# Performance work log

Hardware: AMD Instinct MI355X
Metric: run time of the kernel (lower is better)

The kernel has to match this reference:

```python
import jax, jax.numpy as jnp
import numpy as np

B, F, H, C, K = 4096, 1536, 256, 38, 7  # nodes, feat_dim(effnet_b3), hidden, classes, knn k
EPS = 1e-5  # BatchNorm eps


def setup_inputs() -> dict:
    key = jax.random.key(0)
    ks = jax.random.split(key, 20)
    r = lambda i, shape, s=1.0: jax.random.normal(ks[i], shape, jnp.float32) * s
    u = lambda i, shape: jax.random.uniform(ks[i], shape, jnp.float32, 0.5, 1.5)
    inp = {
        "features": r(0, (B, F)),          # CNN backbone output
        "noise": r(1, (B, B)),             # tie-break noise (scaled by 1e-6 inside)
        # BatchNorm1d on CNN features (eval mode: running stats)
        "bnf_g": jnp.ones((F,)), "bnf_b": jnp.zeros((F,)),
        "bnf_m": r(2, (F,), 0.1), "bnf_v": u(3, (F,)),
        # GCNConv weights
        "W1": r(4, (F, H), 0.02), "b1": jnp.zeros((H,)),
        "W2": r(5, (H, H), 0.05), "b2": jnp.zeros((H,)),
        "W3": r(6, (H, H), 0.05), "b3": jnp.zeros((H,)),
        # PyG BatchNorms (eval mode)
        "bn1_g": jnp.ones((H,)), "bn1_b": jnp.zeros((H,)), "bn1_m": r(7, (H,), 0.1), "bn1_v": u(8, (H,)),
        "bn2_g": jnp.ones((H,)), "bn2_b": jnp.zeros((H,)), "bn2_m": r(9, (H,), 0.1), "bn2_v": u(10, (H,)),
        "bn3_g": jnp.ones((H,)), "bn3_b": jnp.zeros((H,)), "bn3_m": r(11, (H,), 0.1), "bn3_v": u(12, (H,)),
        # classifier MLP
        "Wc1": r(13, (H + F, H // 2), 0.02), "bc1": jnp.zeros((H // 2,)),
        "Wc2": r(14, (H // 2, C), 0.05), "bc2": jnp.zeros((C,)),
    }
    return inp


def _bn(x, g, b, m, v):
    return (x - m) * jax.lax.rsqrt(v + EPS) * g + b


def _knn_edges(x, noise):
    # torch.cdist (p=2) + 1e-6 noise + topk smallest; drop self (col 0)
    sq = jnp.sum(x * x, axis=1)
    d2 = jnp.maximum(sq[:, None] + sq[None, :] - 2.0 * (x @ x.T), 0.0)
    d = jnp.sqrt(d2) + noise * 1e-6
    _, idx = jax.lax.top_k(-d, K + 1)          # smallest K+1 distances
    knn = idx[:, 1:]                           # [B, K] neighbors (col 0 = self)
    src = jnp.repeat(jnp.arange(B), K)         # edge i -> j as in edge_list [[i, j]]
    dst = knn.reshape(-1)
    return src, dst


def _gcn(x, src, dst, W, b):
    # GCNConv: add self-loops, symmetric normalization, aggregate at target (dst)
    h = x @ W
    loop = jnp.arange(B)
    s = jnp.concatenate([src, loop])
    t = jnp.concatenate([dst, loop])
    deg = jnp.zeros((B,), x.dtype).at[t].add(1.0)
    dinv = jax.lax.rsqrt(deg)                  # deg >= 1 due to self-loops
    norm = dinv[s] * dinv[t]
    out = jnp.zeros_like(h).at[t].add(norm[:, None] * h[s])
    return out + b


def reference(features, noise, bnf_g, bnf_b, bnf_m, bnf_v,
              W1, b1, W2, b2, W3, b3,
              bn1_g, bn1_b, bn1_m, bn1_v,
              bn2_g, bn2_b, bn2_m, bn2_v,
              bn3_g, bn3_b, bn3_m, bn3_v,
              Wc1, bc1, Wc2, bc2):
    # CNN head: BN (eval) + dropout(identity in eval)
    x = _bn(features, bnf_g, bnf_b, bnf_m, bnf_v)
    src, dst = _knn_edges(jax.lax.stop_gradient(x), noise)
    x_orig = x
    h = jax.nn.relu(_bn(_gcn(x, src, dst, W1, b1), bn1_g, bn1_b, bn1_m, bn1_v))
    h = jax.nn.relu(_bn(_gcn(h, src, dst, W2, b2), bn2_g, bn2_b, bn2_m, bn2_v))
    h = _bn(_gcn(h, src, dst, W3, b3), bn3_g, bn3_b, bn3_m, bn3_v)
    # batch = arange(B) => global_mean_pool is identity per node
    comb = jnp.concatenate([h, x_orig], axis=1)        # [B, H+F]
    hid = jax.nn.relu(comb @ Wc1 + bc1)
    return hid @ Wc2 + bc2                             # [B, num_classes]
```

## Files before the change

### kernel.cpp

```cpp
#include <hip/hip_runtime.h>
#include <hip/hip_bf16.h>
#include <math.h>

#define Bn 4096
#define Fn 1536
#define Hn 256
#define Cn 38
#define Kn 7
#define GBK 64

typedef __attribute__((ext_vector_type(8))) short short8;
typedef __attribute__((ext_vector_type(4))) float f32x4;
typedef unsigned long long u64;
typedef unsigned int u32;
typedef unsigned short u16;

__device__ __forceinline__ void gld16(const void* g, void* l) {
  __builtin_amdgcn_global_load_lds((const __attribute__((address_space(1))) unsigned int*)g,
                                   (__attribute__((address_space(3))) unsigned int*)l, 16, 0, 0);
}

__global__ void k_prep(const float* __restrict__ g, const float* __restrict__ b,
                       const float* __restrict__ m, const float* __restrict__ v,
                       double* __restrict__ A64, double* __restrict__ C64) {
  int f = blockIdx.x * 256 + threadIdx.x;
  if (f < Fn) {
    double rs = 1.0 / sqrt((double)v[f] + 1e-5);
    double a = (double)g[f] * rs;
    A64[f] = a;
    C64[f] = (double)b[f] - (double)m[f] * a;
  }
}

__global__ void k_bnsplit(const float* __restrict__ feat, const double* __restrict__ A64,
                          const double* __restrict__ C64,
                          u16* __restrict__ Ah, u16* __restrict__ Al) {
  int row = blockIdx.x;
  int f0 = threadIdx.x * 8;
  const float* fr = feat + (size_t)row * Fn + f0;
  float4 a = *reinterpret_cast<const float4*>(fr);
  float4 b = *reinterpret_cast<const float4*>(fr + 4);
  float xs[8] = {a.x, a.y, a.z, a.w, b.x, b.y, b.z, b.w};
  short8 hv, lv;
#pragma unroll
  for (int k = 0; k < 8; k++) {
    float x = (float)fma((double)xs[k], A64[f0 + k], C64[f0 + k]);
    __hip_bfloat16 h = __float2bfloat16(x);
    float hf = __bfloat162float(h);
    __hip_bfloat16 lo = __float2bfloat16(x - hf);
    hv[k] = (short)*reinterpret_cast<u16*>(&h);
    lv[k] = (short)*reinterpret_cast<u16*>(&lo);
  }
  *reinterpret_cast<short8*>(Ah + (size_t)row * Fn + f0) = hv;
  *reinterpret_cast<short8*>(Al + (size_t)row * Fn + f0) = lv;
}

__global__ void k_rowsq(const float* __restrict__ feat, const double* __restrict__ A64,
                        const double* __restrict__ C64, double* __restrict__ sq) {
  int row = blockIdx.x, tid = threadIdx.x;
  const float* fr = feat + (size_t)row * Fn;
  double s = 0.0;
  for (int f = tid; f < Fn; f += 256) {
    double x = fma((double)fr[f], A64[f], C64[f]);
    s += x * x;
  }
  for (int o = 32; o > 0; o >>= 1) s += __shfl_down(s, o);
  __shared__ double red[4];
  if ((tid & 63) == 0) red[tid >> 6] = s;
  __syncthreads();
  if (tid == 0) sq[row] = red[0] + red[1] + red[2] + red[3];
}

__global__ void k_wsplit(const float* __restrict__ W, int K, int N,
                         u16* __restrict__ Wth, u16* __restrict__ Wtl) {
  __shared__ float t[32][33];
  int k0 = blockIdx.y * 32, n0 = blockIdx.x * 32;
  int tx = threadIdx.x & 31, ty = threadIdx.x >> 5;
  for (int p = 0; p < 32; p += 8) {
    int k = k0 + ty + p, n = n0 + tx;
    t[ty + p][tx] = (k < K && n < N) ? W[(size_t)k * N + n] : 0.f;
  }
  __syncthreads();
  for (int p = 0; p < 32; p += 8) {
    int n = n0 + ty + p, k = k0 + tx;
    if (n < N && k < K) {
      float x = t[tx][ty + p];
      __hip_bfloat16 h = __float2bfloat16(x);
      float hf = __bfloat162float(h);
      __hip_bfloat16 lo = __float2bfloat16(x - hf);
      Wth[(size_t)n * K + k] = *reinterpret_cast<u16*>(&h);
      Wtl[(size_t)n * K + k] = *reinterpret_cast<u16*>(&lo);
    }
  }
}

__global__ __launch_bounds__(256) void k_gram(
    const u16* __restrict__ Ah, const double* __restrict__ sq, u64* __restrict__ part) {
  __shared__ union {
    u16 t[2][8192];
    float c2[128 * 65];
  } lds;
  const int tid = threadIdx.x;
  const int w = tid >> 6, l = tid & 63;
  int swz = (blockIdx.x & 7) * 66 + (blockIdx.x >> 3);
  int rem = swz, ti = 0;
#pragma unroll 1
  while (rem >= 32 - ti) { rem -= 32 - ti; ti++; }
  const int tj = ti + rem;
  const int rA0 = ti * 128, rB0 = tj * 128;
  const int isDiag = (ti == tj);

  f32x4 acc[4][4];
  const f32x4 fz = {0.f, 0.f, 0.f, 0.f};
#pragma unroll
  for (int i = 0; i < 4; i++)
#pragma unroll
    for (int j = 0; j < 4; j++) acc[i][j] = fz;

  const u16* mats[2] = { Ah + (size_t)rA0 * Fn, Ah + (size_t)rB0 * Fn };

  auto stage = [&](int k0) {
#pragma unroll
    for (int q = 0; q < 8; q++) {
      int idx = w * 8 + q;
      int mm = idx >> 4, kh = (idx >> 3) & 1, s = idx & 7;
      int row = s * 16 + (l >> 2);
      int colel = ((l & 3) * 8) ^ ((row & 8) ? 16 : 0);
      gld16(mats[mm] + (size_t)row * Fn + k0 + kh * 32 + colel,
            (char*)&lds.t[mm][0] + kh * 8192 + s * 1024);
    }
  };

  const int swzr = (l & 8) ? 32 : 0;
  const int cB = ((l >> 4) * 16) ^ swzr;

  stage(0);
  const int NT = Fn / GBK;
  for (int kt = 0; kt < NT; kt++) {
    __syncthreads();
#pragma unroll
    for (int kh = 0; kh < 2; kh++) {
      short8 fa[4], fb[4];
#pragma unroll
      for (int i = 0; i < 4; i++) {
        int ar = (w >> 1) * 64 + i * 16 + (l & 15);
        fa[i] = *reinterpret_cast<const short8*>((const char*)&lds.t[0][0] + kh * 8192 + ar * 64 + cB);
        int br = (w & 1) * 64 + i * 16 + (l & 15);
        fb[i] = *reinterpret_cast<const short8*>((const char*)&lds.t[1][0] + kh * 8192 + br * 64 + cB);
      }
#pragma unroll
      for (int i = 0; i < 4; i++)
#pragma unroll
        for (int j = 0; j < 4; j++)
          acc[i][j] = __builtin_amdgcn_mfma_f32_16x16x32_bf16(fa[i], fb[j], acc[i][j], 0, 0, 0);
    }
    __syncthreads();
    if (kt + 1 < NT) stage((kt + 1) * GBK);
  }

  const int fr = l & 15, fq = l >> 4;
#pragma unroll 1
  for (int p = 0; p < 2; p++) {
    if ((w & 1) == p) {
#pragma unroll
      for (int i = 0; i < 4; i++) {
        int r0 = (w >> 1) * 64 + i * 16 + fq * 4;
#pragma unroll
        for (int j = 0; j < 4; j++) {
          int c0 = j * 16 + fr;
#pragma unroll
          for (int gg = 0; gg < 4; gg++)
            lds.c2[(r0 + gg) * 65 + c0] = acc[i][j][gg];
        }
      }
    }
    __syncthreads();
    u64 top[8];
#pragma unroll
    for (int k = 0; k < 8; k++) top[k] = ~0ull;
    int prow = -1, slot = 0;
    if (tid < 128) {
      int grow = rA0 + tid;
      float sqr = (float)sq[grow];
#pragma unroll 1
      for (int c = 0; c < 64; c++) {
        int gc = rB0 + p * 64 + c;
        if (gc == grow) continue;
        float gv = lds.c2[tid * 65 + c];
        float d2 = fmaxf(sqr + (float)sq[gc] - 2.f * gv, 0.f);
        u64 key = ((u64)__float_as_uint(d2) << 32) | (u32)gc;
        if (key < top[7]) {
          top[7] = key;
#pragma unroll
          for (int k = 7; k > 0; k--)
            if (top[k] < top[k - 1]) { u64 tmp = top[k]; top[k] = top[k - 1]; top[k - 1] = tmp; }
        }
      }
      prow = grow; slot = tj * 2 + p;
    } else if (!isDiag) {
      int idx = tid - 128, cl = idx >> 1, q = idx & 1;
      int gcol = rB0 + p * 64 + cl;
      float sqc = (float)sq[gcol];
#pragma unroll 1
      for (int s = 0; s < 64; s++) {
        int rr = q * 64 + s;
        float gv = lds.c2[rr * 65 + cl];
        int gr = rA0 + rr;
        float d2 = fmaxf(sqc + (float)sq[gr] - 2.f * gv, 0.f);
        u64 key = ((u64)__float_as_uint(d2) << 32) | (u32)gr;
        if (key < top[7]) {
          top[7] = key;
#pragma unroll
          for (int k = 7; k > 0; k--)
            if (top[k] < top[k - 1]) { u64 tmp = top[k]; top[k] = top[k - 1]; top[k - 1] = tmp; }
        }
      }
      prow = gcol; slot = ti * 2 + q;
    }
    if (prow >= 0) {
      u64* dst = part + ((size_t)prow * 64 + slot) * 8;
#pragma unroll
      for (int k = 0; k < 8; k++) dst[k] = top[k];
    }
    __syncthreads();
  }
}

__global__ __launch_bounds__(256) void k_candmerge(const u64* __restrict__ part,
                                                   int* __restrict__ cand) {
  int row = blockIdx.x * 4 + (threadIdx.x >> 6);
  int l = threadIdx.x & 63;
  const u64* p = part + (size_t)row * 512 + (size_t)l * 8;
  u64 e[8];
#pragma unroll
  for (int k = 0; k < 8; k++) e[k] = p[k];
#pragma unroll 1
  for (int rnd = 0; rnd < 16; rnd++) {
    u64 m = e[0];
#pragma unroll
    for (int k = 1; k < 8; k++) m = e[k] < m ? e[k] : m;
#pragma unroll
    for (int off = 32; off; off >>= 1) {
      u64 o = __shfl_xor(m, off);
      m = o < m ? o : m;
    }
    if (l == 0) cand[row * 16 + rnd] = (int)(u32)m;
#pragma unroll
    for (int k = 0; k < 8; k++)
      if (e[k] == m) e[k] = ~0ull;
  }
}

__global__ __launch_bounds__(256) void k_rerank(
    const float* __restrict__ feat, const double* __restrict__ A64,
    const double* __restrict__ C64, const double* __restrict__ sq,
    const float* __restrict__ noise, const int* __restrict__ cand,
    int* __restrict__ knn, float* __restrict__ deg) {
  int row = blockIdx.x;
  int w = threadIdx.x >> 6, l = threadIdx.x & 63;
  double xr[Fn / 64];
  const float* fr = feat + (size_t)row * Fn;
#pragma unroll
  for (int i = 0; i < Fn / 64; i++) {
    int e = l + 64 * i;
    xr[i] = fma((double)fr[e], A64[e], C64[e]);
  }
  __shared__ double dots[16];
  for (int m = w; m < 16; m += 4) {
    int c = cand[row * 16 + m];
    const float* fc = feat + (size_t)c * Fn;
    double s = 0.0;
#pragma unroll
    for (int i = 0; i < Fn / 64; i++) {
      int e = l + 64 * i;
      double xj = fma((double)fc[e], A64[e], C64[e]);
      s = fma(xr[i], xj, s);
    }
#pragma unroll
    for (int off = 32; off; off >>= 1) s += __shfl_xor(s, off);
    if (l == 0) dots[m] = s;
  }
  __syncthreads();
  if (threadIdx.x == 0) {
    double sr = sq[row];
    double bd[Kn]; int bi7[Kn];
#pragma unroll
    for (int k = 0; k < Kn; k++) { bd[k] = 1e300; bi7[k] = 0; }
#pragma unroll 1
    for (int m = 0; m < 16; m++) {
      int c = cand[row * 16 + m];
      double d2 = sr + sq[c] - 2.0 * dots[m];
      d2 = d2 > 0.0 ? d2 : 0.0;
      double d = sqrt(d2) + (double)noise[(size_t)row * Bn + c] * 1e-6;
      if (d < bd[Kn - 1]) {
        bd[Kn - 1] = d; bi7[Kn - 1] = c;
#pragma unroll
        for (int k = Kn - 1; k > 0; k--)
          if (bd[k] < bd[k - 1]) {
            double td = bd[k]; bd[k] = bd[k - 1]; bd[k - 1] = td;
            int ti = bi7[k]; bi7[k] = bi7[k - 1]; bi7[k - 1] = ti;
          }
      }
    }
#pragma unroll
    for (int k = 0; k < Kn; k++) {
      knn[row * Kn + k] = bi7[k];
      atomicAdd(&deg[bi7[k]], 1.f);
    }
  }
}

__global__ void k_deginit(float* __restrict__ deg) {
  int i = blockIdx.x * 256 + threadIdx.x;
  if (i < Bn) deg[i] = 1.f;
}
__global__ void k_dinv(const float* __restrict__ deg, float* __restrict__ dinv) {
  int i = blockIdx.x * 256 + threadIdx.x;
  if (i < Bn) dinv[i] = rsqrtf(deg[i]);
}

__global__ void k_aggsc(const float* __restrict__ h, const int* __restrict__ knn,
                        const float* __restrict__ dinv, float* __restrict__ out) {
  int s = blockIdx.x, f = threadIdx.x;
  float hv = h[(size_t)s * Hn + f] * dinv[s];
#pragma unroll
  for (int k = 0; k < Kn; k++) {
    int t = knn[s * Kn + k];
    atomicAdd(&out[(size_t)t * Hn + f], dinv[t] * hv);
  }
}

__global__ void k_bnact_split(const float* __restrict__ x, const float* __restrict__ g,
                              const float* __restrict__ b, const float* __restrict__ m,
                              const float* __restrict__ v, int relu,
                              u16* __restrict__ oh, u16* __restrict__ ol) {
  size_t i8 = ((size_t)blockIdx.x * 256 + threadIdx.x) * 8;
  int c0 = (int)(i8 & (Hn - 1));
  float4 a = *reinterpret_cast<const float4*>(x + i8);
  float4 bb = *reinterpret_cast<const float4*>(x + i8 + 4);
  float xs[8] = {a.x, a.y, a.z, a.w, bb.x, bb.y, bb.z, bb.w};
  short8 hv, lv;
#pragma unroll
  for (int k = 0; k < 8; k++) {
    int c = c0 + k;
    float val = (xs[k] - m[c]) * rsqrtf(v[c] + 1e-5f) * g[c] + b[c];
    if (relu) val = fmaxf(val, 0.f);
    __hip_bfloat16 h = __float2bfloat16(val);
    float hf = __bfloat162float(h);
    __hip_bfloat16 lo = __float2bfloat16(val - hf);
    hv[k] = (short)*reinterpret_cast<u16*>(&h);
    lv[k] = (short)*reinterpret_cast<u16*>(&lo);
  }
  *reinterpret_cast<short8*>(oh + i8) = hv;
  *reinterpret_cast<short8*>(ol + i8) = lv;
}

__global__ __launch_bounds__(256) void k_mgemm(
    const u16* __restrict__ Ah1, const u16* __restrict__ Al1, int lda1,
    const u16* __restrict__ Ah2, const u16* __restrict__ Al2, int lda2, int Ksplit,
    const u16* __restrict__ Wth, const u16* __restrict__ Wtl,
    const float* __restrict__ bias, float* __restrict__ C, int N, int K, int ep,
    float* __restrict__ C2, const float* __restrict__ dinvp) {
  __shared__ u16 tA[2][4096];
  __shared__ u16 tB[2][4096];
  const int tid = threadIdx.x;
  const int w = tid >> 6, l = tid & 63;
  const int m0 = blockIdx.y * 64, n0 = blockIdx.x * 64;
  const int fr = l & 15, fq = l >> 4;

  f32x4 acc[2][2];
  const f32x4 fz = {0.f, 0.f, 0.f, 0.f};
#pragma unroll
  for (int i = 0; i < 2; i++)
#pragma unroll
    for (int j = 0; j < 2; j++) acc[i][j] = fz;

  auto stage = [&](int k0) {
#pragma unroll
    for (int q = 0; q < 2; q++) {
      int s = w * 2 + q;
      int kg = k0 + s * 8;
      const u16* ah; const u16* al; int ld; int kk = kg;
      if (kg < Ksplit) { ah = Ah1; al = Al1; ld = lda1; }
      else             { ah = Ah2; al = Al2; ld = lda2; kk = kg - Ksplit; }
      gld16(ah + (size_t)(m0 + l) * ld + kk, (char*)&tA[0][0] + s * 1024);
      gld16(al + (size_t)(m0 + l) * ld + kk, (char*)&tA[1][0] + s * 1024);
      gld16(Wth + (size_t)(n0 + l) * K + kg, (char*)&tB[0][0] + s * 1024);
      gld16(Wtl + (size_t)(n0 + l) * K + kg, (char*)&tB[1][0] + s * 1024);
    }
  };

  stage(0);
  const int NT = K / GBK;
  for (int kt = 0; kt < NT; kt++) {
    __syncthreads();
#pragma unroll
    for (int kh = 0; kh < 2; kh++) {
      const int kb = (kh * 4 + fq) * 1024;
      short8 fa[2][2], fb[2][2];
#pragma unroll
      for (int i = 0; i < 2; i++) {
        int ar = (w >> 1) * 32 + i * 16 + fr;
        fa[0][i] = *reinterpret_cast<const short8*>((const char*)&tA[0][0] + kb + ar * 16);
        fa[1][i] = *reinterpret_cast<const short8*>((const char*)&tA[1][0] + kb + ar * 16);
        int br = (w & 1) * 32 + i * 16 + fr;
        fb[0][i] = *reinterpret_cast<const short8*>((const char*)&tB[0][0] + kb + br * 16);
        fb[1][i] = *reinterpret_cast<const short8*>((const char*)&tB[1][0] + kb + br * 16);
      }
#pragma unroll
      for (int i = 0; i < 2; i++)
#pragma unroll
        for (int j = 0; j < 2; j++) {
          acc[i][j] = __builtin_amdgcn_mfma_f32_16x16x32_bf16(fa[1][i], fb[0][j], acc[i][j], 0, 0, 0);
          acc[i][j] = __builtin_amdgcn_mfma_f32_16x16x32_bf16(fa[0][i], fb[1][j], acc[i][j], 0, 0, 0);
          acc[i][j] = __builtin_amdgcn_mfma_f32_16x16x32_bf16(fa[0][i], fb[0][j], acc[i][j], 0, 0, 0);
        }
    }
    __syncthreads();
    if (kt + 1 < NT) stage((kt + 1) * GBK);
  }

#pragma unroll
  for (int i = 0; i < 2; i++) {
    int rg0 = m0 + (w >> 1) * 32 + i * 16 + fq * 4;
#pragma unroll
    for (int j = 0; j < 2; j++) {
      int cg = n0 + (w & 1) * 32 + j * 16 + fr;
      float bv = (ep >= 1) ? bias[cg] : 0.f;
#pragma unroll
      for (int g = 0; g < 4; g++) {
        float raw = acc[i][j][g];
        size_t idx = (size_t)(rg0 + g) * N + cg;
        if (ep == 3) {
          float di = dinvp[rg0 + g];
          C[idx] = raw;
          C2[idx] = di * di * raw + bv;
        } else {
          float val = raw + bv;
          if (ep == 2) val = fmaxf(val, 0.f);
          C[idx] = val;
        }
      }
    }
  }
}

__global__ __launch_bounds__(256) void k_gemm(
    const float* __restrict__ A1, int lda1,
    const float* __restrict__ Bw, const float* __restrict__ bias,
    float* __restrict__ C, int M, int N, int K, int ep) {
  __shared__ float As[16][65];
  __shared__ float Bs[16][64];
  int tid = threadIdx.x;
  int n0 = blockIdx.x * 64;
  int row0 = blockIdx.y * 64;
  int tx = tid & 15, ty = tid >> 4;
  float acc[4][4] = {};
  for (int k0 = 0; k0 < K; k0 += 16) {
    int kk = tid & 15, mi = tid >> 4;
#pragma unroll
    for (int p = 0; p < 4; p++) {
      int row = row0 + mi + p * 16;
      As[kk][mi + p * 16] = A1[(size_t)row * lda1 + k0 + kk];
    }
    int nj = tid & 63, kq = tid >> 6;
#pragma unroll
    for (int p = 0; p < 4; p++) {
      int kb = kq + p * 4;
      int n = n0 + nj;
      Bs[kb][nj] = (n < N) ? Bw[(size_t)(k0 + kb) * N + n] : 0.f;
    }
    __syncthreads();
#pragma unroll
    for (int kk2 = 0; kk2 < 16; kk2++) {
      float a[4], b[4];
#pragma unroll
      for (int i = 0; i < 4; i++) a[i] = As[kk2][ty * 4 + i];
#pragma unroll
      for (int j = 0; j < 4; j++) b[j] = Bs[kk2][tx * 4 + j];
#pragma unroll
      for (int i = 0; i < 4; i++)
#pragma unroll
        for (int j = 0; j < 4; j++) acc[i][j] += a[i] * b[j];
    }
    __syncthreads();
  }
#pragma unroll
  for (int i = 0; i < 4; i++) {
    int row = row0 + ty * 4 + i;
#pragma unroll
    for (int j = 0; j < 4; j++) {
      int n = n0 + tx * 4 + j;
      if (n < N) {
        float v = acc[i][j];
        if (ep >= 1) v += bias[n];
        if (ep == 2) v = fmaxf(v, 0.f);
        C[(size_t)row * N + n] = v;
      }
    }
  }
}

extern "C" void kernel_launch(void* const* d_in, const int* in_sizes, int n_in,
                              void* d_out, int out_size, void* d_ws, size_t ws_size,
                              hipStream_t stream) {
  const float* feat  = (const float*)d_in[0];
  const float* noise = (const float*)d_in[1];
  const float* bnf_g = (const float*)d_in[2];
  const float* bnf_b = (const float*)d_in[3];
  const float* bnf_m = (const float*)d_in[4];
  const float* bnf_v = (const float*)d_in[5];
  const float* W1 = (const float*)d_in[6];
  const float* b1 = (const float*)d_in[7];
  const float* W2 = (const float*)d_in[8];
  const float* b2 = (const float*)d_in[9];
  const float* W3 = (const float*)d_in[10];
  const float* b3 = (const float*)d_in[11];
  const float* bn1_g = (const float*)d_in[12];
  const float* bn1_b = (const float*)d_in[13];
  const float* bn1_m = (const float*)d_in[14];
  const float* bn1_v = (const float*)d_in[15];
  const float* bn2_g = (const float*)d_in[16];
  const float* bn2_b = (const float*)d_in[17];
  const float* bn2_m = (const float*)d_in[18];
  const float* bn2_v = (const float*)d_in[19];
  const float* bn3_g = (const float*)d_in[20];
  const float* bn3_b = (const float*)d_in[21];
  const float* bn3_m = (const float*)d_in[22];
  const float* bn3_v = (const float*)d_in[23];
  const float* Wc1 = (const float*)d_in[24];
  const float* bc1 = (const float*)d_in[25];
  const float* Wc2 = (const float*)d_in[26];
  const float* bc2 = (const float*)d_in[27];
  float* outp = (float*)d_out;

  char* w = (char*)d_ws;
  size_t off = 0;
  auto alloc = [&](size_t n) { void* p = w + off; off = (off + n + 255) & ~(size_t)255; return p; };
  u16*    Ahb  = (u16*)   alloc((size_t)Bn * Fn * 2);
  u16*    Alb  = (u16*)   alloc((size_t)Bn * Fn * 2);
  double* A64  = (double*)alloc(Fn * 8);
  double* C64  = (double*)alloc(Fn * 8);
  double* sq   = (double*)alloc(Bn * 8);
  u64*    part = (u64*)   alloc((size_t)Bn * 64 * 8 * 8);
  int*    cand = (int*)   alloc((size_t)Bn * 16 * 4);
  int*    knn  = (int*)   alloc((size_t)Bn * Kn * 4);
  float*  deg  = (float*) alloc(Bn * 4);
  float*  dinv = (float*) alloc(Bn * 4);
  float*  g1   = (float*) alloc((size_t)Bn * Hn * 4);
  float*  g2   = (float*) alloc((size_t)Bn * Hn * 4);
  float*  hid  = (float*) alloc((size_t)Bn * 128 * 4);
  u16*    sh   = (u16*)   alloc((size_t)Bn * Hn * 2);
  u16*    sl   = (u16*)   alloc((size_t)Bn * Hn * 2);
  u16*    W1th = (u16*)   alloc((size_t)Fn * Hn * 2);
  u16*    W1tl = (u16*)   alloc((size_t)Fn * Hn * 2);
  u16*    W2th = (u16*)   alloc((size_t)Hn * Hn * 2);
  u16*    W2tl = (u16*)   alloc((size_t)Hn * Hn * 2);
  u16*    W3th = (u16*)   alloc((size_t)Hn * Hn * 2);
  u16*    W3tl = (u16*)   alloc((size_t)Hn * Hn * 2);
  u16*    Wc1th= (u16*)   alloc((size_t)(Hn + Fn) * 128 * 2);
  u16*    Wc1tl= (u16*)   alloc((size_t)(Hn + Fn) * 128 * 2);
  (void)ws_size; (void)in_sizes; (void)n_in; (void)out_size;

  k_prep<<<(Fn + 255) / 256, 256, 0, stream>>>(bnf_g, bnf_b, bnf_m, bnf_v, A64, C64);
  k_bnsplit<<<Bn, Fn / 8, 0, stream>>>(feat, A64, C64, Ahb, Alb);
  k_rowsq<<<Bn, 256, 0, stream>>>(feat, A64, C64, sq);
  k_wsplit<<<dim3(Hn / 32, Fn / 32), 256, 0, stream>>>(W1, Fn, Hn, W1th, W1tl);
  k_wsplit<<<dim3(Hn / 32, Hn / 32), 256, 0, stream>>>(W2, Hn, Hn, W2th, W2tl);
  k_wsplit<<<dim3(Hn / 32, Hn / 32), 256, 0, stream>>>(W3, Hn, Hn, W3th, W3tl);
  k_wsplit<<<dim3(128 / 32, (Hn + Fn) / 32), 256, 0, stream>>>(Wc1, Hn + Fn, 128, Wc1th, Wc1tl);

  k_gram<<<528, 256, 0, stream>>>(Ahb, sq, part);
  k_candmerge<<<Bn / 4, 256, 0, stream>>>(part, cand);
  k_deginit<<<(Bn + 255) / 256, 256, 0, stream>>>(deg);
  k_rerank<<<Bn, 256, 0, stream>>>(feat, A64, C64, sq, noise, cand, knn, deg);
  k_dinv<<<(Bn + 255) / 256, 256, 0, stream>>>(deg, dinv);

  dim3 gm(Hn / 64, Bn / 64);
  k_mgemm<<<gm, 256, 0, stream>>>(Ahb, Alb, Fn, Ahb, Alb, Fn, Fn, W1th, W1tl, b1, g1, Hn, Fn, 3, g2, dinv);
  k_aggsc<<<Bn, Hn, 0, stream>>>(g1, knn, dinv, g2);
  k_bnact_split<<<(Bn * Hn) / (256 * 8), 256, 0, stream>>>(g2, bn1_g, bn1_b, bn1_m, bn1_v, 1, sh, sl);
  k_mgemm<<<gm, 256, 0, stream>>>(sh, sl, Hn, sh, sl, Hn, Hn, W2th, W2tl, b2, g1, Hn, Hn, 3, g2, dinv);
  k_aggsc<<<Bn, Hn, 0, stream>>>(g1, knn, dinv, g2);
  k_bnact_split<<<(Bn * Hn) / (256 * 8), 256, 0, stream>>>(g2, bn2_g, bn2_b, bn2_m, bn2_v, 1, sh, sl);
  k_mgemm<<<gm, 256, 0, stream>>>(sh, sl, Hn, sh, sl, Hn, Hn, W3th, W3tl, b3, g1, Hn, Hn, 3, g2, dinv);
  k_aggsc<<<Bn, Hn, 0, stream>>>(g1, knn, dinv, g2);
  k_bnact_split<<<(Bn * Hn) / (256 * 8), 256, 0, stream>>>(g2, bn3_g, bn3_b, bn3_m, bn3_v, 0, sh, sl);
  k_mgemm<<<dim3(128 / 64, Bn / 64), 256, 0, stream>>>(sh, sl, Hn, Ahb, Alb, Fn, Hn,
                                                       Wc1th, Wc1tl, bc1, hid, 128, Hn + Fn, 2,
                                                       nullptr, nullptr);
  k_gemm<<<dim3(1, Bn / 64), 256, 0, stream>>>(hid, 128, Wc2, bc2, outp, Bn, Cn, 128, 1);
}
```

Baseline: 586.6 us.

## Double-buffer GEMM LDS tiles, fuse row norms into BN split, MFMA final classifier

Gram and split-bf16 GEMM kernels now use two LDS buffers, issuing the next tile's global-to-LDS loads before computing the current one and dropping one barrier per k-step. The row squared-norm pass is folded into the BN/bf16 split kernel, removing a separate full read of the features. The final classifier layer moves from a scalar fp32 GEMM to the MFMA split-bf16 GEMM, with the hidden layer's epilogue emitting hi/lo bf16 directly. This doubles LDS use per block, which may lower occupancy.

Result: slower. 614.9 us (+4.8%).

```diff
diff --git a/kernel.cpp b/kernel.cpp
--- a/kernel.cpp
+++ b/kernel.cpp
@@ -34,7 +34,7 @@
 
 __global__ void k_bnsplit(const float* __restrict__ feat, const double* __restrict__ A64,
                           const double* __restrict__ C64,
-                          u16* __restrict__ Ah, u16* __restrict__ Al) {
+                          u16* __restrict__ Ah, u16* __restrict__ Al, double* __restrict__ sq) {
   int row = blockIdx.x;
   int f0 = threadIdx.x * 8;
   const float* fr = feat + (size_t)row * Fn + f0;
@@ -42,9 +42,12 @@
   float4 b = *reinterpret_cast<const float4*>(fr + 4);
   float xs[8] = {a.x, a.y, a.z, a.w, b.x, b.y, b.z, b.w};
   short8 hv, lv;
+  double ss = 0.0;
 #pragma unroll
   for (int k = 0; k < 8; k++) {
-    float x = (float)fma((double)xs[k], A64[f0 + k], C64[f0 + k]);
+    double xd = fma((double)xs[k], A64[f0 + k], C64[f0 + k]);
+    ss = fma(xd, xd, ss);
+    float x = (float)xd;
     __hip_bfloat16 h = __float2bfloat16(x);
     float hf = __bfloat162float(h);
     __hip_bfloat16 lo = __float2bfloat16(x - hf);
@@ -53,22 +56,12 @@
   }
   *reinterpret_cast<short8*>(Ah + (size_t)row * Fn + f0) = hv;
   *reinterpret_cast<short8*>(Al + (size_t)row * Fn + f0) = lv;
-}
-
-__global__ void k_rowsq(const float* __restrict__ feat, const double* __restrict__ A64,
-                        const double* __restrict__ C64, double* __restrict__ sq) {
-  int row = blockIdx.x, tid = threadIdx.x;
-  const float* fr = feat + (size_t)row * Fn;
-  double s = 0.0;
-  for (int f = tid; f < Fn; f += 256) {
-    double x = fma((double)fr[f], A64[f], C64[f]);
-    s += x * x;
-  }
-  for (int o = 32; o > 0; o >>= 1) s += __shfl_down(s, o);
-  __shared__ double red[4];
-  if ((tid & 63) == 0) red[tid >> 6] = s;
+#pragma unroll
+  for (int o = 32; o; o >>= 1) ss += __shfl_down(ss, o);
+  __shared__ double red[3];
+  if ((threadIdx.x & 63) == 0) red[threadIdx.x >> 6] = ss;
   __syncthreads();
-  if (tid == 0) sq[row] = red[0] + red[1] + red[2] + red[3];
+  if (threadIdx.x == 0) sq[row] = red[0] + red[1] + red[2];
 }
 
 __global__ void k_wsplit(const float* __restrict__ W, int K, int N,
@@ -97,7 +90,7 @@
 __global__ __launch_bounds__(256) void k_gram(
     const u16* __restrict__ Ah, const double* __restrict__ sq, u64* __restrict__ part) {
   __shared__ union {
-    u16 t[2][8192];
+    u16 t[2][2][8192];
     float c2[128 * 65];
   } lds;
   const int tid = threadIdx.x;
@@ -119,7 +112,7 @@
 
   const u16* mats[2] = { Ah + (size_t)rA0 * Fn, Ah + (size_t)rB0 * Fn };
 
-  auto stage = [&](int k0) {
+  auto stage = [&](int buf, int k0) {
 #pragma unroll
     for (int q = 0; q < 8; q++) {
       int idx = w * 8 + q;
@@ -127,26 +120,28 @@
       int row = s * 16 + (l >> 2);
       int colel = ((l & 3) * 8) ^ ((row & 8) ? 16 : 0);
       gld16(mats[mm] + (size_t)row * Fn + k0 + kh * 32 + colel,
-            (char*)&lds.t[mm][0] + kh * 8192 + s * 1024);
+            (char*)&lds.t[buf][mm][0] + kh * 8192 + s * 1024);
     }
   };
 
   const int swzr = (l & 8) ? 32 : 0;
   const int cB = ((l >> 4) * 16) ^ swzr;
 
-  stage(0);
+  stage(0, 0);
   const int NT = Fn / GBK;
+  int cur = 0;
   for (int kt = 0; kt < NT; kt++) {
     __syncthreads();
+    if (kt + 1 < NT) stage(cur ^ 1, (kt + 1) * GBK);
 #pragma unroll
     for (int kh = 0; kh < 2; kh++) {
       short8 fa[4], fb[4];
 #pragma unroll
       for (int i = 0; i < 4; i++) {
         int ar = (w >> 1) * 64 + i * 16 + (l & 15);
-        fa[i] = *reinterpret_cast<const short8*>((const char*)&lds.t[0][0] + kh * 8192 + ar * 64 + cB);
+        fa[i] = *reinterpret_cast<const short8*>((const char*)&lds.t[cur][0][0] + kh * 8192 + ar * 64 + cB);
         int br = (w & 1) * 64 + i * 16 + (l & 15);
-        fb[i] = *reinterpret_cast<const short8*>((const char*)&lds.t[1][0] + kh * 8192 + br * 64 + cB);
+        fb[i] = *reinterpret_cast<const short8*>((const char*)&lds.t[cur][1][0] + kh * 8192 + br * 64 + cB);
       }
 #pragma unroll
       for (int i = 0; i < 4; i++)
@@ -154,9 +149,9 @@
         for (int j = 0; j < 4; j++)
           acc[i][j] = __builtin_amdgcn_mfma_f32_16x16x32_bf16(fa[i], fb[j], acc[i][j], 0, 0, 0);
     }
-    __syncthreads();
-    if (kt + 1 < NT) stage((kt + 1) * GBK);
-  }
+    cur ^= 1;
+  }
+  __syncthreads();
 
   const int fr = l & 15, fq = l >> 4;
 #pragma unroll 1
@@ -360,9 +355,10 @@
     const u16* __restrict__ Ah2, const u16* __restrict__ Al2, int lda2, int Ksplit,
     const u16* __restrict__ Wth, const u16* __restrict__ Wtl,
     const float* __restrict__ bias, float* __restrict__ C, int N, int K, int ep,
-    float* __restrict__ C2, const float* __restrict__ dinvp) {
-  __shared__ u16 tA[2][4096];
-  __shared__ u16 tB[2][4096];
+    float* __restrict__ C2, const float* __restrict__ dinvp,
+    u16* __restrict__ OH, u16* __restrict__ OL) {
+  __shared__ u16 tA[2][2][4096];
+  __shared__ u16 tB[2][2][4096];
   const int tid = threadIdx.x;
   const int w = tid >> 6, l = tid & 63;
   const int m0 = blockIdx.y * 64, n0 = blockIdx.x * 64;
@@ -375,7 +371,7 @@
 #pragma unroll
     for (int j = 0; j < 2; j++) acc[i][j] = fz;
 
-  auto stage = [&](int k0) {
+  auto stage = [&](int buf, int k0) {
 #pragma unroll
     for (int q = 0; q < 2; q++) {
       int s = w * 2 + q;
@@ -383,17 +379,19 @@
       const u16* ah; const u16* al; int ld; int kk = kg;
       if (kg < Ksplit) { ah = Ah1; al = Al1; ld = lda1; }
       else             { ah = Ah2; al = Al2; ld = lda2; kk = kg - Ksplit; }
-      gld16(ah + (size_t)(m0 + l) * ld + kk, (char*)&tA[0][0] + s * 1024);
-      gld16(al + (size_t)(m0 + l) * ld + kk, (char*)&tA[1][0] + s * 1024);
-      gld16(Wth + (size_t)(n0 + l) * K + kg, (char*)&tB[0][0] + s * 1024);
-      gld16(Wtl + (size_t)(n0 + l) * K + kg, (char*)&tB[1][0] + s * 1024);
+      gld16(ah + (size_t)(m0 + l) * ld + kk, (char*)&tA[buf][0][0] + s * 1024);
+      gld16(al + (size_t)(m0 + l) * ld + kk, (char*)&tA[buf][1][0] + s * 1024);
+      gld16(Wth + (size_t)(n0 + l) * K + kg, (char*)&tB[buf][0][0] + s * 1024);
+      gld16(Wtl + (size_t)(n0 + l) * K + kg, (char*)&tB[buf][1][0] + s * 1024);
     }
   };
 
-  stage(0);
+  stage(0, 0);
   const int NT = K / GBK;
+  int cur = 0;
   for (int kt = 0; kt < NT; kt++) {
     __syncthreads();
+    if (kt + 1 < NT) stage(cur ^ 1, (kt + 1) * GBK);
 #pragma unroll
     for (int kh = 0; kh < 2; kh++) {
       const int kb = (kh * 4 + fq) * 1024;
@@ -401,11 +399,11 @@
 #pragma unroll
       for (int i = 0; i < 2; i++) {
         int ar = (w >> 1) * 32 + i * 16 + fr;
-        fa[0][i] = *reinterpret_cast<const short8*>((const char*)&tA[0][0] + kb + ar * 16);
-        fa[1][i] = *reinterpret_cast<const short8*>((const char*)&tA[1][0] + kb + ar * 16);
+        fa[0][i] = *reinterpret_cast<const short8*>((const char*)&tA[cur][0][0] + kb + ar * 16);
+        fa[1][i] = *reinterpret_cast<const short8*>((const char*)&tA[cur][1][0] + kb + ar * 16);
         int br = (w & 1) * 32 + i * 16 + fr;
-        fb[0][i] = *reinterpret_cast<const short8*>((const char*)&tB[0][0] + kb + br * 16);
-        fb[1][i] = *reinterpret_cast<const short8*>((const char*)&tB[1][0] + kb + br * 16);
+        fb[0][i] = *reinterpret_cast<const short8*>((const char*)&tB[cur][0][0] + kb + br * 16);
+        fb[1][i] = *reinterpret_cast<const short8*>((const char*)&tB[cur][1][0] + kb + br * 16);
       }
 #pragma unroll
       for (int i = 0; i < 2; i++)
@@ -416,8 +414,7 @@
           acc[i][j] = __builtin_amdgcn_mfma_f32_16x16x32_bf16(fa[0][i], fb[0][j], acc[i][j], 0, 0, 0);
         }
     }
-    __syncthreads();
-    if (kt + 1 < NT) stage((kt + 1) * GBK);
+    cur ^= 1;
   }
 
 #pragma unroll
@@ -426,6 +423,7 @@
 #pragma unroll
     for (int j = 0; j < 2; j++) {
       int cg = n0 + (w & 1) * 32 + j * 16 + fr;
+      if (cg >= N) continue;
       float bv = (ep >= 1) ? bias[cg] : 0.f;
 #pragma unroll
       for (int g = 0; g < 4; g++) {
@@ -435,67 +433,18 @@
           float di = dinvp[rg0 + g];
           C[idx] = raw;
           C2[idx] = di * di * raw + bv;
+        } else if (ep == 4) {
+          float val = fmaxf(raw + bv, 0.f);
+          __hip_bfloat16 h = __float2bfloat16(val);
+          float hf = __bfloat162float(h);
+          __hip_bfloat16 lo = __float2bfloat16(val - hf);
+          OH[idx] = *reinterpret_cast<u16*>(&h);
+          OL[idx] = *reinterpret_cast<u16*>(&lo);
         } else {
           float val = raw + bv;
           if (ep == 2) val = fmaxf(val, 0.f);
           C[idx] = val;
         }
-      }
-    }
-  }
-}
-
-__global__ __launch_bounds__(256) void k_gemm(
-    const float* __restrict__ A1, int lda1,
-    const float* __restrict__ Bw, const float* __restrict__ bias,
-    float* __restrict__ C, int M, int N, int K, int ep) {
-  __shared__ float As[16][65];
-  __shared__ float Bs[16][64];
-  int tid = threadIdx.x;
-  int n0 = blockIdx.x * 64;
-  int row0 = blockIdx.y * 64;
-  int tx = tid & 15, ty = tid >> 4;
-  float acc[4][4] = {};
-  for (int k0 = 0; k0 < K; k0 += 16) {
-    int kk = tid & 15, mi = tid >> 4;
-#pragma unroll
-    for (int p = 0; p < 4; p++) {
-      int row = row0 + mi + p * 16;
-      As[kk][mi + p * 16] = A1[(size_t)row * lda1 + k0 + kk];
-    }
-    int nj = tid & 63, kq = tid >> 6;
-#pragma unroll
-    for (int p = 0; p < 4; p++) {
-      int kb = kq + p * 4;
-      int n = n0 + nj;
-      Bs[kb][nj] = (n < N) ? Bw[(size_t)(k0 + kb) * N + n] : 0.f;
-    }
-    __syncthreads();
-#pragma unroll
-    for (int kk2 = 0; kk2 < 16; kk2++) {
-      float a[4], b[4];
-#pragma unroll
-      for (int i = 0; i < 4; i++) a[i] = As[kk2][ty * 4 + i];
-#pragma unroll
-      for (int j = 0; j < 4; j++) b[j] = Bs[kk2][tx * 4 + j];
-#pragma unroll
-      for (int i = 0; i < 4; i++)
-#pragma unroll
-        for (int j = 0; j < 4; j++) acc[i][j] += a[i] * b[j];
-    }
-    __syncthreads();
-  }
-#pragma unroll
-  for (int i = 0; i < 4; i++) {
-    int row = row0 + ty * 4 + i;
-#pragma unroll
-    for (int j = 0; j < 4; j++) {
-      int n = n0 + tx * 4 + j;
-      if (n < N) {
-        float v = acc[i][j];
-        if (ep >= 1) v += bias[n];
-        if (ep == 2) v = fmaxf(v, 0.f);
-        C[(size_t)row * N + n] = v;
       }
     }
   }
@@ -549,9 +498,10 @@
   float*  dinv = (float*) alloc(Bn * 4);
   float*  g1   = (float*) alloc((size_t)Bn * Hn * 4);
   float*  g2   = (float*) alloc((size_t)Bn * Hn * 4);
-  float*  hid  = (float*) alloc((size_t)Bn * 128 * 4);
   u16*    sh   = (u16*)   alloc((size_t)Bn * Hn * 2);
   u16*    sl   = (u16*)   alloc((size_t)Bn * Hn * 2);
+  u16*    hidh = (u16*)   alloc((size_t)Bn * 128 * 2);
+  u16*    hidl = (u16*)   alloc((size_t)Bn * 128 * 2);
   u16*    W1th = (u16*)   alloc((size_t)Fn * Hn * 2);
   u16*    W1tl = (u16*)   alloc((size_t)Fn * Hn * 2);
   u16*    W2th = (u16*)   alloc((size_t)Hn * Hn * 2);
@@ -560,15 +510,17 @@
   u16*    W3tl = (u16*)   alloc((size_t)Hn * Hn * 2);
   u16*    Wc1th= (u16*)   alloc((size_t)(Hn + Fn) * 128 * 2);
   u16*    Wc1tl= (u16*)   alloc((size_t)(Hn + Fn) * 128 * 2);
+  u16*    Wc2th= (u16*)   alloc((size_t)64 * 128 * 2);
+  u16*    Wc2tl= (u16*)   alloc((size_t)64 * 128 * 2);
   (void)ws_size; (void)in_sizes; (void)n_in; (void)out_size;
 
   k_prep<<<(Fn + 255) / 256, 256, 0, stream>>>(bnf_g, bnf_b, bnf_m, bnf_v, A64, C64);
-  k_bnsplit<<<Bn, Fn / 8, 0, stream>>>(feat, A64, C64, Ahb, Alb);
-  k_rowsq<<<Bn, 256, 0, stream>>>(feat, A64, C64, sq);
+  k_bnsplit<<<Bn, Fn / 8, 0, stream>>>(feat, A64, C64, Ahb, Alb, sq);
   k_wsplit<<<dim3(Hn / 32, Fn / 32), 256, 0, stream>>>(W1, Fn, Hn, W1th, W1tl);
   k_wsplit<<<dim3(Hn / 32, Hn / 32), 256, 0, stream>>>(W2, Hn, Hn, W2th, W2tl);
   k_wsplit<<<dim3(Hn / 32, Hn / 32), 256, 0, stream>>>(W3, Hn, Hn, W3th, W3tl);
   k_wsplit<<<dim3(128 / 32, (Hn + Fn) / 32), 256, 0, stream>>>(Wc1, Hn + Fn, 128, Wc1th, Wc1tl);
+  k_wsplit<<<dim3(2, 4), 256, 0, stream>>>(Wc2, 128, Cn, Wc2th, Wc2tl);
 
   k_gram<<<528, 256, 0, stream>>>(Ahb, sq, part);
   k_candmerge<<<Bn / 4, 256, 0, stream>>>(part, cand);
@@ -577,17 +529,22 @@
   k_dinv<<<(Bn + 255) / 256, 256, 0, stream>>>(deg, dinv);
 
   dim3 gm(Hn / 64, Bn / 64);
-  k_mgemm<<<gm, 256, 0, stream>>>(Ahb, Alb, Fn, Ahb, Alb, Fn, Fn, W1th, W1tl, b1, g1, Hn, Fn, 3, g2, dinv);
+  k_mgemm<<<gm, 256, 0, stream>>>(Ahb, Alb, Fn, Ahb, Alb, Fn, Fn, W1th, W1tl, b1, g1, Hn, Fn, 3,
+                                  g2, dinv, nullptr, nullptr);
   k_aggsc<<<Bn, Hn, 0, stream>>>(g1, knn, dinv, g2);
   k_bnact_split<<<(Bn * Hn) / (256 * 8), 256, 0, stream>>>(g2, bn1_g, bn1_b, bn1_m, bn1_v, 1, sh, sl);
-  k_mgemm<<<gm, 256, 0, stream>>>(sh, sl, Hn, sh, sl, Hn, Hn, W2th, W2tl, b2, g1, Hn, Hn, 3, g2, dinv);
+  k_mgemm<<<gm, 256, 0, stream>>>(sh, sl, Hn, sh, sl, Hn, Hn, W2th, W2tl, b2, g1, Hn, Hn, 3,
+                                  g2, dinv, nullptr, nullptr);
   k_aggsc<<<Bn, Hn, 0, stream>>>(g1, knn, dinv, g2);
   k_bnact_split<<<(Bn * Hn) / (256 * 8), 256, 0, stream>>>(g2, bn2_g, bn2_b, bn2_m, bn2_v, 1, sh, sl);
-  k_mgemm<<<gm, 256, 0, stream>>>(sh, sl, Hn, sh, sl, Hn, Hn, W3th, W3tl, b3, g1, Hn, Hn, 3, g2, dinv);
+  k_mgemm<<<gm, 256, 0, stream>>>(sh, sl, Hn, sh, sl, Hn, Hn, W3th, W3tl, b3, g1, Hn, Hn, 3,
+                                  g2, dinv, nullptr, nullptr);
   k_aggsc<<<Bn, Hn, 0, stream>>>(g1, knn, dinv, g2);
   k_bnact_split<<<(Bn * Hn) / (256 * 8), 256, 0, stream>>>(g2, bn3_g, bn3_b, bn3_m, bn3_v, 0, sh, sl);
   k_mgemm<<<dim3(128 / 64, Bn / 64), 256, 0, stream>>>(sh, sl, Hn, Ahb, Alb, Fn, Hn,
-                                                       Wc1th, Wc1tl, bc1, hid, 128, Hn + Fn, 2,
-                                                       nullptr, nullptr);
-  k_gemm<<<dim3(1, Bn / 64), 256, 0, stream>>>(hid, 128, Wc2, bc2, outp, Bn, Cn, 128, 1);
-}
+                                                       Wc1th, Wc1tl, bc1, nullptr, 128, Hn + Fn, 4,
+                                                       nullptr, nullptr, hidh, hidl);
+  k_mgemm<<<dim3(1, Bn / 64), 256, 0, stream>>>(hidh, hidl, 128, hidh, hidl, 128, 128,
+                                                Wc2th, Wc2tl, bc2, outp, Cn, 128, 1,
+                                                nullptr, nullptr, nullptr, nullptr);
+}
```
